# Optimization experiments

Hardware: AMD Instinct MI355X
Metric: run time of the kernel (lower is better)

## Reference

```python
import jax, jax.numpy as jnp
import numpy as np

D = 1024
H = 16
HD = D // H
L = 2048
B = 1
MLP = 8192
ROPE_BASE = 10000.0
LN_EPS = 1e-5


def layer_norm(x):
    mu = jnp.mean(x, axis=-1, keepdims=True)
    var = jnp.var(x, axis=-1, keepdims=True)
    return (x - mu) / jnp.sqrt(var + LN_EPS)


def rope(x):
    # x: [B, H, L, HD]; non-traditional (rotate-half / NeoX style)
    half = HD // 2
    inv_freq = 1.0 / (ROPE_BASE ** (jnp.arange(0, half, dtype=jnp.float32) / half))
    pos = jnp.arange(x.shape[2], dtype=jnp.float32)
    ang = pos[:, None] * inv_freq[None, :]            # [L, half]
    cos, sin = jnp.cos(ang), jnp.sin(ang)
    x1, x2 = x[..., :half], x[..., half:]
    return jnp.concatenate([x1 * cos - x2 * sin, x2 * cos + x1 * sin], axis=-1).astype(x.dtype)


def setup_inputs() -> dict:
    key = jax.random.key(0)
    ks = jax.random.split(key, 5)
    x = jax.random.normal(ks[0], (B, L, D), dtype=jnp.float32)
    # causal additive mask
    neg = jnp.finfo(jnp.float32).min
    mask = jnp.where(jnp.tril(jnp.ones((L, L), dtype=bool)), 0.0, neg).astype(jnp.float32)
    W_attn = jax.random.normal(ks[1], (3 * D, D), dtype=jnp.float32) * (D ** -0.5)
    W_out = jax.random.normal(ks[2], (D, D), dtype=jnp.float32) * (D ** -0.5)
    W_ffp = jax.random.normal(ks[3], (MLP, D), dtype=jnp.float32) * (D ** -0.5)
    W_ffo = jax.random.normal(ks[4], (D, MLP // 2), dtype=jnp.float32) * ((MLP // 2) ** -0.5)
    return {"x": x, "mask": mask, "W_attn": W_attn, "W_out": W_out, "W_ffp": W_ffp, "W_ffo": W_ffo}


def block(x, mask, W_attn, W_out, W_ffp, W_ffo):
    b, l, d = x.shape
    scale = HD ** -0.5
    # attention branch
    xn = layer_norm(x)
    qkv = xn @ W_attn.T                                    # [B, L, 3D]
    q, k, v = jnp.split(qkv, 3, axis=-1)
    q = q.reshape(b, l, H, HD).transpose(0, 2, 1, 3)       # [B, H, L, HD]
    k = k.reshape(b, l, H, HD).transpose(0, 2, 1, 3)
    v = v.reshape(b, l, H, HD).transpose(0, 2, 1, 3)
    q = rope(q)
    k = rope(k)
    scores = jnp.einsum('bhqd,bhkd->bhqk', q * scale, k)   # [B, H, L, L]
    scores = scores + mask
    probs = jax.nn.softmax(scores.astype(jnp.float32), axis=-1).astype(scores.dtype)
    attn = jnp.einsum('bhqk,bhkd->bhqd', probs, v)
    attn = attn.transpose(0, 2, 1, 3).reshape(b, l, d)
    r = attn @ W_out.T
    h = x + r
    # SwiGLU MLP branch: split ff_proj output, swiglu(x2, x1) = silu(x2) * x1
    g = layer_norm(h) @ W_ffp.T                            # [B, L, MLP]
    x1, x2 = jnp.split(g, 2, axis=-1)
    mlp = (jax.nn.silu(x2) * x1) @ W_ffo.T
    return h + mlp


def reference(x, mask, W_attn, W_out, W_ffp, W_ffo):
    return block(x, mask, W_attn, W_out, W_ffp, W_ffo)
```

## Files before the change

### kernel.cpp

```cpp
#include <hip/hip_runtime.h>
#include <math.h>

#define DMODEL 1024
#define NHEAD  16
#define HDIM   64
#define SEQ    2048
#define MLPD   8192
#define HALF_MLP 4096
static constexpr float LN_EPS_C = 1e-5f;
#define NEG_BIG (-1e30f)
#define SM_SHIFT 16.0f

typedef short bf16x8 __attribute__((ext_vector_type(8)));
typedef float f32x4  __attribute__((ext_vector_type(4)));

__device__ __forceinline__ unsigned short f2b(float f) {
    unsigned int u = __float_as_uint(f);
    u = (u + 0x7FFFu + ((u >> 16) & 1u)) >> 16;
    return (unsigned short)u;
}
__device__ __forceinline__ float b2f(unsigned short h) {
    return __uint_as_float((unsigned int)h << 16);
}

__device__ __forceinline__ void async_copy16(const unsigned short* g, unsigned short* l) {
    __builtin_amdgcn_global_load_lds(
        (const __attribute__((address_space(1))) unsigned int*)(g),
        (__attribute__((address_space(3))) unsigned int*)(l),
        16, 0, 0);
}

__global__ void prep_all(const float* __restrict__ x,
                         const float* __restrict__ W_attn, const float* __restrict__ W_out,
                         const float* __restrict__ W_ffp,  const float* __restrict__ W_ffo,
                         unsigned short* __restrict__ xnb, float2* __restrict__ ct,
                         unsigned short* __restrict__ oa, unsigned short* __restrict__ ob,
                         unsigned short* __restrict__ oc, unsigned short* __restrict__ od) {
    const int bid = blockIdx.x;
    const int tid = threadIdx.x;
    if (bid < SEQ) {
        __shared__ float rs[256], rs2[256];
        float4 v = *(const float4*)(x + (size_t)bid * DMODEL + tid * 4);
        rs[tid]  = v.x + v.y + v.z + v.w;
        rs2[tid] = v.x * v.x + v.y * v.y + v.z * v.z + v.w * v.w;
        __syncthreads();
        for (int off = 128; off > 0; off >>= 1) {
            if (tid < off) { rs[tid] += rs[tid + off]; rs2[tid] += rs2[tid + off]; }
            __syncthreads();
        }
        float mu  = rs[0] * (1.0f / DMODEL);
        float var = rs2[0] * (1.0f / DMODEL) - mu * mu;
        float inv = rsqrtf(var + LN_EPS_C);
        ushort4 o;
        o.x = f2b((v.x - mu) * inv); o.y = f2b((v.y - mu) * inv);
        o.z = f2b((v.z - mu) * inv); o.w = f2b((v.w - mu) * inv);
        *(ushort4*)(xnb + (size_t)bid * DMODEL + tid * 4) = o;
    } else if (bid < SEQ + 256) {
        int idx = (bid - SEQ) * 256 + tid;
        int pos = idx >> 5, p = idx & 31;
        float invf = powf(10000.0f, -(float)p / 32.0f);
        float ang = (float)pos * invf;
        ct[idx] = make_float2(cosf(ang), sinf(ang));
    } else {
        const int n1 = 3 * DMODEL * DMODEL;
        const int n2 = n1 + DMODEL * DMODEL;
        const int n3 = n2 + MLPD * DMODEL;
        int i = ((bid - SEQ - 256) * 256 + tid) * 4;
        const float* src; unsigned short* dst; int off;
        if (i < n1)      { src = W_attn; dst = oa; off = i; }
        else if (i < n2) { src = W_out;  dst = ob; off = i - n1; }
        else if (i < n3) {
            src = W_ffp; off = i - n2;
            int row = off >> 10, col = off & 1023;
            int rp  = (row < HALF_MLP) ? (2 * row) : (2 * (row - HALF_MLP) + 1);
            float4 v = *(const float4*)(src + off);
            ushort4 o;
            o.x = f2b(v.x); o.y = f2b(v.y); o.z = f2b(v.z); o.w = f2b(v.w);
            *(ushort4*)(oc + ((size_t)rp << 10) + col) = o;
            return;
        }
        else             { src = W_ffo; dst = od; off = i - n3; }
        float4 v = *(const float4*)(src + off);
        ushort4 o;
        o.x = f2b(v.x); o.y = f2b(v.y); o.z = f2b(v.z); o.w = f2b(v.w);
        *(ushort4*)(dst + off) = o;
    }
}

__global__ void ln_red2(const float* __restrict__ p0, const float* __restrict__ p1,
                        const float* __restrict__ x, float* __restrict__ h,
                        unsigned short* __restrict__ xnb) {
    const int row = blockIdx.x;
    const int tid = threadIdx.x;
    __shared__ float rs[256], rs2[256];
    const size_t base = (size_t)row * DMODEL + tid * 4;
    float4 a = *(const float4*)(p0 + base);
    float4 b = *(const float4*)(p1 + base);
    float4 r = *(const float4*)(x + base);
    float4 v = { a.x + b.x + r.x, a.y + b.y + r.y, a.z + b.z + r.z, a.w + b.w + r.w };
    *(float4*)(h + base) = v;
    rs[tid]  = v.x + v.y + v.z + v.w;
    rs2[tid] = v.x * v.x + v.y * v.y + v.z * v.z + v.w * v.w;
    __syncthreads();
    for (int off = 128; off > 0; off >>= 1) {
        if (tid < off) { rs[tid] += rs[tid + off]; rs2[tid] += rs2[tid + off]; }
        __syncthreads();
    }
    float mu  = rs[0] * (1.0f / DMODEL);
    float var = rs2[0] * (1.0f / DMODEL) - mu * mu;
    float inv = rsqrtf(var + LN_EPS_C);
    ushort4 o;
    o.x = f2b((v.x - mu) * inv); o.y = f2b((v.y - mu) * inv);
    o.z = f2b((v.z - mu) * inv); o.w = f2b((v.w - mu) * inv);
    *(ushort4*)(xnb + base) = o;
}

__global__ __launch_bounds__(256)
void gemm_qkv(const unsigned short* __restrict__ A, const unsigned short* __restrict__ B,
              const float2* __restrict__ ct,
              unsigned short* __restrict__ Qp, unsigned short* __restrict__ Kp,
              unsigned short* __restrict__ Vt) {
    __shared__ unsigned short As[128 * 32];
    __shared__ unsigned short Bs[128 * 32];
    __shared__ unsigned short St[4][16][72];
    const int tid  = threadIdx.x;
    const int lane = tid & 63;
    const int w    = tid >> 6;
    const int wm   = w >> 1;
    const int wn   = w & 1;
    const int m0   = blockIdx.y * 128;
    const int n0   = blockIdx.x * 128;

    f32x4 acc[4][4] = {};

    const int srow = lane >> 2;
    const int scol = (lane & 3) * 8;
    const unsigned short* Abase = A + (size_t)(m0 + w * 32 + srow) * DMODEL + scol;
    const unsigned short* Bbase = B + (size_t)(n0 + w * 32 + srow) * DMODEL + scol;
    unsigned short* AsW = &As[(w * 32) * 32];
    unsigned short* BsW = &Bs[(w * 32) * 32];

    const int fr = lane & 15;
    const int fk = (lane >> 4) * 8;

    for (int k0 = 0; k0 < DMODEL; k0 += 32) {
        async_copy16(Abase + k0,               AsW);
        async_copy16(Abase + k0 + 16 * DMODEL, AsW + 16 * 32);
        async_copy16(Bbase + k0,               BsW);
        async_copy16(Bbase + k0 + 16 * DMODEL, BsW + 16 * 32);
        __syncthreads();

        bf16x8 af[4], bfr[4];
#pragma unroll
        for (int i = 0; i < 4; ++i)
            af[i] = *(const bf16x8*)(&As[(wm * 64 + i * 16 + fr) * 32 + fk]);
#pragma unroll
        for (int j = 0; j < 4; ++j)
            bfr[j] = *(const bf16x8*)(&Bs[(wn * 64 + j * 16 + fr) * 32 + fk]);
#pragma unroll
        for (int i = 0; i < 4; ++i)
#pragma unroll
            for (int j = 0; j < 4; ++j)
                acc[i][j] = __builtin_amdgcn_mfma_f32_16x16x32_bf16(af[i], bfr[j], acc[i][j], 0, 0, 0);
        __syncthreads();
    }

    const int erow   = (lane >> 4) * 4;
    const int ecol   = lane & 15;
    const int region = blockIdx.x >> 3;
    const int head   = ((n0 + wn * 64) >> 6) & 15;

    if (region == 2) {
        const int sbase = m0 + wm * 64;
        const int dl = lane >> 3;
        const int ch = (lane & 7) * 8;
#pragma unroll
        for (int j = 0; j < 4; ++j) {
#pragma unroll
            for (int i = 0; i < 4; ++i) {
                ushort4 o;
                o.x = f2b(acc[i][j][0]); o.y = f2b(acc[i][j][1]);
                o.z = f2b(acc[i][j][2]); o.w = f2b(acc[i][j][3]);
                *(ushort4*)&St[w][ecol][i * 16 + erow] = o;
            }
#pragma unroll
            for (int p = 0; p < 2; ++p) {
                const int dd = p * 8 + dl;
                bf16x8 v = *(const bf16x8*)&St[w][dd][ch];
                *(bf16x8*)(Vt + ((size_t)head * HDIM + j * 16 + dd) * SEQ + sbase + ch) = v;
            }
        }
    } else {
        unsigned short* P = region ? Kp : Qp;
        const float scale = region ? 1.0f : 0.125f;
        unsigned short* qb = &St[w][erow][0];
#pragma unroll
        for (int i = 0; i < 4; ++i) {
#pragma unroll
            for (int r = 0; r < 4; ++r) {
                const int rowg = m0 + wm * 64 + i * 16 + erow + r;
                const float2* crow = ct + (size_t)rowg * 32;
#pragma unroll
                for (int jj = 0; jj < 2; ++jj) {
                    const float2 cs = crow[jj * 16 + ecol];
                    const float x1 = acc[i][jj][r];
                    const float x2 = acc[i][jj + 2][r];
                    qb[jj * 16 + ecol]      = f2b((x1 * cs.x - x2 * cs.y) * scale);
                    qb[jj * 16 + ecol + 32] = f2b((x2 * cs.x + x1 * cs.y) * scale);
                }
                ushort4 o = *(const ushort4*)&qb[ecol * 4];
                *(ushort4*)(P + ((size_t)head * SEQ + rowg) * HDIM + ecol * 4) = o;
            }
        }
    }
}

__global__ __launch_bounds__(256, 2)
void gemm_mfma_sk(const unsigned short* __restrict__ A, const unsigned short* __restrict__ B,
                  float* __restrict__ P, int Ksub, int lda, int ldb, int ldc) {
    __shared__ __align__(16) unsigned short U[4][2][128 * 32];
    const int tid  = threadIdx.x;
    const int lane = tid & 63;
    const int w    = tid >> 6;
    const int wm   = w >> 1;
    const int wn   = w & 1;
    const int m0   = blockIdx.y * 128;
    const int n0   = blockIdx.x * 128;
    const int kb   = blockIdx.z * Ksub;

    f32x4 acc[4][4] = {};

    const int srow = lane >> 2;
    const int scg  = ((lane & 3) ^ ((lane >> 3) & 3)) * 8;
    const int fr   = lane & 15;
    const int quad = lane >> 4;
    const int rchunk = (quad ^ ((fr >> 1) & 3)) * 8;

#define SK_STAGE(T)                                                           \
    {                                                                         \
        const int kk_ = kb + (T) * 32;                                        \
        const int sl_ = (T) & 3;                                              \
        const unsigned short* ga_ = A + (size_t)(m0 + w * 32 + srow) * lda + kk_ + scg; \
        const unsigned short* gb_ = B + (size_t)(n0 + w * 32 + srow) * ldb + kk_ + scg; \
        unsigned short* la_ = &U[sl_][0][(w * 32) * 32];                      \
        unsigned short* lb_ = &U[sl_][1][(w * 32) * 32];                      \
        async_copy16(ga_,                    la_);                            \
        async_copy16(ga_ + 16 * (size_t)lda, la_ + 16 * 32);                  \
        async_copy16(gb_,                    lb_);                            \
        async_copy16(gb_ + 16 * (size_t)ldb, lb_ + 16 * 32);                  \
    }

    const int NT = Ksub >> 5;
    SK_STAGE(0)
    SK_STAGE(1)
    asm volatile("s_waitcnt vmcnt(4)" ::: "memory");
    __builtin_amdgcn_s_barrier();

    for (int t = 0; t < NT; ++t) {
        if (t + 2 < NT) {
            SK_STAGE(t + 2)
            asm volatile("s_waitcnt vmcnt(8)" ::: "memory");
        } else if (t + 1 < NT) {
            asm volatile("s_waitcnt vmcnt(4)" ::: "memory");
        } else {
            asm volatile("s_waitcnt vmcnt(0)" ::: "memory");
        }
        __builtin_amdgcn_s_barrier();
        __builtin_amdgcn_sched_barrier(0);

        const unsigned short* As_ = &U[t & 3][0][0];
        const unsigned short* Bs_ = &U[t & 3][1][0];
        bf16x8 af[4], bfr[4];
#pragma unroll
        for (int i = 0; i < 4; ++i)
            af[i] = *(const bf16x8*)&As_[(wm * 64 + i * 16 + fr) * 32 + rchunk];
#pragma unroll
        for (int j = 0; j < 4; ++j)
            bfr[j] = *(const bf16x8*)&Bs_[(wn * 64 + j * 16 + fr) * 32 + rchunk];

        __builtin_amdgcn_s_setprio(1);
#pragma unroll
        for (int i = 0; i < 4; ++i)
#pragma unroll
            for (int j = 0; j < 4; ++j)
                acc[i][j] = __builtin_amdgcn_mfma_f32_16x16x32_bf16(af[i], bfr[j], acc[i][j], 0, 0, 0);
        __builtin_amdgcn_s_setprio(0);
    }
#undef SK_STAGE

    float* Pp = P + (size_t)blockIdx.z * SEQ * ldc;
    const int erow = (lane >> 4) * 4;
    const int ecol = lane & 15;
#pragma unroll
    for (int i = 0; i < 4; ++i)
#pragma unroll
        for (int j = 0; j < 4; ++j) {
            const int colg = n0 + wn * 64 + j * 16 + ecol;
#pragma unroll
            for (int r = 0; r < 4; ++r) {
                const int rowg = m0 + wm * 64 + i * 16 + erow + r;
                Pp[(size_t)rowg * ldc + colg] = acc[i][j][r];
            }
        }
}

__global__ void reduce4_kernel(const float* __restrict__ p0, const float* __restrict__ p1,
                               const float* __restrict__ p2, const float* __restrict__ p3,
                               const float* __restrict__ res, float* __restrict__ out) {
    int i = (blockIdx.x * blockDim.x + threadIdx.x) * 4;
    float4 a = *(const float4*)(p0 + i);
    float4 b = *(const float4*)(p1 + i);
    float4 c = *(const float4*)(p2 + i);
    float4 d = *(const float4*)(p3 + i);
    float4 r = *(const float4*)(res + i);
    float4 o = { a.x + b.x + c.x + d.x + r.x, a.y + b.y + c.y + d.y + r.y,
                 a.z + b.z + c.z + d.z + r.z, a.w + b.w + c.w + d.w + r.w };
    *(float4*)(out + i) = o;
}

#define FT  32
#define FNT (DMODEL / FT)
__global__ __launch_bounds__(512, 2)
void gemm_ffp_silu_p(const unsigned short* __restrict__ A,
                     const unsigned short* __restrict__ B,
                     unsigned short* __restrict__ gact) {
    __shared__ __align__(16) unsigned short U[4][2][256 * 32];
    const int tid  = threadIdx.x;
    const int lane = tid & 63;
    const int w    = tid >> 6;
    const int wm   = w >> 2;
    const int wn   = w & 3;
    const int fr   = lane & 15;
    const int quad = lane >> 4;

    const int sid = (blockIdx.x & 7) * 32 + (blockIdx.x >> 3);
    const int tm  = sid & 7;
    const int tn  = sid >> 3;

    const unsigned short* Ag = A + (size_t)(tm * 256) * DMODEL;
    const unsigned short* Bg = B + (size_t)(tn * 256) * DMODEL;

    const int srow = tid >> 2;
    const int scg  = ((tid & 3) ^ ((tid >> 3) & 3)) * 8;
    unsigned short* lba = (unsigned short*)&U[0][0][0] + w * 512;
    unsigned short* lbb = (unsigned short*)&U[0][1][0] + w * 512;

    const int rchunk = (quad ^ ((fr >> 1) & 3)) * 8;

    f32x4 acc[8][4] = {};

#define FFP_STAGE(T)                                                          \
    {                                                                         \
        const int k0_ = (T) * FT;                                             \
        const int sl_ = (T) & 3;                                              \
        const unsigned short* ga_ = Ag + (size_t)srow * DMODEL + k0_ + scg;   \
        const unsigned short* gb_ = Bg + (size_t)srow * DMODEL + k0_ + scg;   \
        unsigned short* la_ = lba + sl_ * 16384;                              \
        unsigned short* lb_ = lbb + sl_ * 16384;                              \
        async_copy16(ga_,                la_);                                \
        async_copy16(ga_ + 128 * DMODEL, la_ + 4096);                         \
        async_copy16(gb_,                lb_);                                \
        async_copy16(gb_ + 128 * DMODEL, lb_ + 4096);                         \
    }

    FFP_STAGE(0)
    FFP_STAGE(1)
    asm volatile("s_waitcnt vmcnt(4)" ::: "memory");
    __builtin_amdgcn_s_barrier();

    for (int t = 0; t < FNT; ++t) {
        if (t + 2 < FNT) {
            FFP_STAGE(t + 2)
            asm volatile("s_waitcnt vmcnt(8)" ::: "memory");
        } else if (t + 1 < FNT) {
            asm volatile("s_waitcnt vmcnt(4)" ::: "memory");
        } else {
            asm volatile("s_waitcnt vmcnt(0)" ::: "memory");
        }
        __builtin_amdgcn_s_barrier();
        __builtin_amdgcn_sched_barrier(0);

        const unsigned short* As_ = &U[t & 3][0][0];
        const unsigned short* Bs_ = &U[t & 3][1][0];
        bf16x8 af[8], bf[4];
#pragma unroll
        for (int i = 0; i < 8; ++i)
            af[i] = *(const bf16x8*)&As_[(wm * 128 + i * 16 + fr) * 32 + rchunk];
#pragma unroll
        for (int j = 0; j < 4; ++j)
            bf[j] = *(const bf16x8*)&Bs_[(wn * 64 + j * 16 + fr) * 32 + rchunk];

        __builtin_amdgcn_s_setprio(1);
#pragma unroll
        for (int i = 0; i < 8; ++i)
#pragma unroll
            for (int j = 0; j < 4; ++j)
                acc[i][j] = __builtin_amdgcn_mfma_f32_16x16x32_bf16(af[i], bf[j], acc[i][j], 0, 0, 0);
        __builtin_amdgcn_s_setprio(0);
    }
#undef FFP_STAGE

    __syncthreads();
    typedef unsigned short StRow[40];
    StRow* Stw = reinterpret_cast<StRow*>(&U[0][0][0]) + (size_t)w * 128;

    const bool evn = (fr & 1) == 0;
#pragma unroll
    for (int i = 0; i < 8; ++i)
#pragma unroll
        for (int j = 0; j < 4; ++j)
#pragma unroll
            for (int r = 0; r < 4; ++r) {
                float own = acc[i][j][r];
                float oth = __shfl_xor(own, 1);
                if (evn) {
                    float sil = oth / (1.0f + __expf(-oth));
                    Stw[i * 16 + quad * 4 + r][j * 8 + (fr >> 1)] = f2b(sil * own);
                }
            }
    {
        const int growb = tm * 256 + wm * 128;
        const int colb  = tn * 128 + wn * 32;
#pragma unroll
        for (int p = 0; p < 2; ++p) {
            const int rl = p * 64 + lane;
            unsigned short* dst = gact + (size_t)(growb + rl) * HALF_MLP + colb;
            bf16x8 v0 = *(const bf16x8*)&Stw[rl][0];
            bf16x8 v1 = *(const bf16x8*)&Stw[rl][8];
            bf16x8 v2 = *(const bf16x8*)&Stw[rl][16];
            bf16x8 v3 = *(const bf16x8*)&Stw[rl][24];
            *(bf16x8*)(dst + 0)  = v0;
            *(bf16x8*)(dst + 8)  = v1;
            *(bf16x8*)(dst + 16) = v2;
            *(bf16x8*)(dst + 24) = v3;
        }
    }
}

__global__ __launch_bounds__(256)
void fattn_blk(const unsigned short* __restrict__ Qp,
               const unsigned short* __restrict__ Kp,
               const unsigned short* __restrict__ Vt,
               unsigned short* __restrict__ out) {
    __shared__ unsigned short Ks[2][64][64];
    __shared__ unsigned short Vs[2][64][64];
    __shared__ unsigned short Ps[4][16][72];
    const int tid  = threadIdx.x;
    const int lane = tid & 63;
    const int w    = tid >> 6;
    const int fr   = lane & 15;
    const int quad = lane >> 4;

    const int f    = blockIdx.x;
    const int head = ((f & 7) << 1) | ((f >> 3) & 1);
    const int ub   = f >> 4;
    const int qb   = (ub & 1) ? (31 - (ub >> 1)) : (ub >> 1);
    const int m0   = qb * 64 + w * 16;

    const unsigned short* Qg = Qp + (size_t)head * SEQ * HDIM;
    const unsigned short* Kg = Kp + (size_t)head * SEQ * HDIM;
    const unsigned short* Vg = Vt + (size_t)head * HDIM * SEQ;

    const int rA = (w << 3) + (lane >> 3);
    const int cg = ((lane & 7) ^ ((lane >> 3) & 7)) << 3;

    bf16x8 qf[2];
#pragma unroll
    for (int kk = 0; kk < 2; ++kk)
        qf[kk] = *(const bf16x8*)(Qg + (size_t)(m0 + fr) * HDIM + kk * 32 + quad * 8);

    bf16x8 ones;
#pragma unroll
    for (int e = 0; e < 8; ++e) ones[e] = (short)0x3F80;

    f32x4 accO[4] = {};
    f32x4 accL = {};

    const int ntiles = qb + 1;

    {
        const unsigned short* gk = Kg + (size_t)rA * HDIM + cg;
        unsigned short* dk = &Ks[0][w << 3][0];
        async_copy16(gk, dk);
        async_copy16(gk + 32 * HDIM, dk + 32 * 64);
        const unsigned short* gv = Vg + (size_t)rA * SEQ + cg;
        unsigned short* dv = &Vs[0][w << 3][0];
        async_copy16(gv, dv);
        async_copy16(gv + 32 * SEQ, dv + 32 * 64);
    }
    __syncthreads();

    int cur = 0;
    for (int t = 0; t < ntiles; ++t) {
        if (t + 1 < ntiles) {
            const int j1 = (t + 1) * 64;
            const unsigned short* gk = Kg + (size_t)(j1 + rA) * HDIM + cg;
            unsigned short* dk = &Ks[cur ^ 1][w << 3][0];
            async_copy16(gk, dk);
            async_copy16(gk + 32 * HDIM, dk + 32 * 64);
            const unsigned short* gv = Vg + (size_t)rA * SEQ + j1 + cg;
            unsigned short* dv = &Vs[cur ^ 1][w << 3][0];
            async_copy16(gv, dv);
            async_copy16(gv + 32 * SEQ, dv + 32 * 64);
        }

        const int j0 = t * 64;
        f32x4 accS[4] = {};
#pragma unroll
        for (int kk = 0; kk < 2; ++kk) {
#pragma unroll
            for (int j = 0; j < 4; ++j) {
                bf16x8 kf = *(const bf16x8*)
                    &Ks[cur][j * 16 + fr][(((kk << 2) + quad) ^ (fr & 7)) << 3];
                accS[j] = __builtin_amdgcn_mfma_f32_16x16x32_bf16(qf[kk], kf, accS[j], 0, 0, 0);
            }
        }

        if (t == ntiles - 1) {
#pragma unroll
            for (int j = 0; j < 4; ++j)
#pragma unroll
                for (int r = 0; r < 4; ++r)
                    if (j0 + j * 16 + fr > m0 + quad * 4 + r) accS[j][r] = NEG_BIG;
        }

#pragma unroll
        for (int j = 0; j < 4; ++j)
#pragma unroll
            for (int r = 0; r < 4; ++r)
                Ps[w][quad * 4 + r][j * 16 + fr] = f2b(__expf(accS[j][r] - SM_SHIFT));

#pragma unroll
        for (int kk = 0; kk < 2; ++kk) {
            bf16x8 pf = *(const bf16x8*)&Ps[w][fr][kk * 32 + quad * 8];
            accL = __builtin_amdgcn_mfma_f32_16x16x32_bf16(pf, ones, accL, 0, 0, 0);
#pragma unroll
            for (int j = 0; j < 4; ++j) {
                bf16x8 vf = *(const bf16x8*)
                    &Vs[cur][j * 16 + fr][(((kk << 2) + quad) ^ (fr & 7)) << 3];
                accO[j] = __builtin_amdgcn_mfma_f32_16x16x32_bf16(pf, vf, accO[j], 0, 0, 0);
            }
        }

        __syncthreads();
        cur ^= 1;
    }

#pragma unroll
    for (int r = 0; r < 4; ++r) {
        const float inv = 1.0f / accL[r];
        const int qrow = m0 + quad * 4 + r;
#pragma unroll
        for (int j = 0; j < 4; ++j)
            out[(size_t)qrow * DMODEL + head * HDIM + j * 16 + fr] = f2b(accO[j][r] * inv);
    }
}

extern "C" void kernel_launch(void* const* d_in, const int* in_sizes, int n_in,
                              void* d_out, int out_size, void* d_ws, size_t ws_size,
                              hipStream_t stream) {
    const float* x      = (const float*)d_in[0];
    const float* W_attn = (const float*)d_in[2];
    const float* W_out  = (const float*)d_in[3];
    const float* W_ffp  = (const float*)d_in[4];
    const float* W_ffo  = (const float*)d_in[5];
    float* out = (float*)d_out;

    char* wsb = (char*)d_ws;
    unsigned short* wb_attn = (unsigned short*)(wsb);
    unsigned short* wb_out  = (unsigned short*)(wsb + (6u  << 20));
    unsigned short* wb_ffp  = (unsigned short*)(wsb + (8u  << 20));
    unsigned short* wb_ffo  = (unsigned short*)(wsb + (24u << 20));
    float*          h       = (float*)(wsb + (32u << 20));
    unsigned short* xnb     = (unsigned short*)(wsb + (40u << 20));
    unsigned short* attnb   = (unsigned short*)(wsb + (44u << 20));
    unsigned short* gact    = (unsigned short*)(wsb + (48u << 20));
    unsigned short* Qp      = (unsigned short*)(wsb + (64u << 20));
    unsigned short* Kp      = (unsigned short*)(wsb + (68u << 20));
    unsigned short* Vt      = (unsigned short*)(wsb + (72u << 20));
    float*          wout_p  = (float*)(wsb + (76u << 20));
    float2*         ct      = (float2*)(wsb + (92u << 20));
    float*          ffo_p   = (float*)(wsb + (64u << 20));

    {
        int f2b_blocks = (3 * DMODEL * DMODEL + DMODEL * DMODEL + MLPD * DMODEL
                          + DMODEL * HALF_MLP) / 4 / 256;
        prep_all<<<SEQ + 256 + f2b_blocks, 256, 0, stream>>>(
            x, W_attn, W_out, W_ffp, W_ffo, xnb, ct,
            wb_attn, wb_out, wb_ffp, wb_ffo);
    }

    gemm_qkv<<<dim3(3 * DMODEL / 128, SEQ / 128), 256, 0, stream>>>(
        xnb, wb_attn, ct, Qp, Kp, Vt);

    fattn_blk<<<512, 256, 0, stream>>>(Qp, Kp, Vt, attnb);

    gemm_mfma_sk<<<dim3(DMODEL / 128, SEQ / 128, 2), 256, 0, stream>>>(
        attnb, wb_out, wout_p, DMODEL / 2, DMODEL, DMODEL, DMODEL);

    ln_red2<<<SEQ, 256, 0, stream>>>(wout_p, wout_p + (size_t)SEQ * DMODEL, x, h, xnb);

    gemm_ffp_silu_p<<<256, 512, 0, stream>>>(xnb, wb_ffp, gact);

    gemm_mfma_sk<<<dim3(DMODEL / 128, SEQ / 128, 4), 256, 0, stream>>>(
        gact, wb_ffo, ffo_p, HALF_MLP / 4, HALF_MLP, HALF_MLP, DMODEL);

    reduce4_kernel<<<SEQ * DMODEL / 4 / 256, 256, 0, stream>>>(
        ffo_p, ffo_p + (size_t)SEQ * DMODEL, ffo_p + 2 * (size_t)SEQ * DMODEL,
        ffo_p + 3 * (size_t)SEQ * DMODEL, h, out);
}
```

Before: 289.7 us.

## Multi-stage async pipeline with swizzled LDS for QKV GEMM

Replaces the single-buffered load/sync/compute loop in the QKV projection GEMM with a 4-slot LDS ring and a prefetch distance of two tiles. Waits now use explicit vmcnt counts and one barrier per iteration instead of two. It also XOR-swizzles the 16-byte chunks in LDS to cut bank conflicts, raises wave priority around the MFMA block, and asks for two blocks per CU through launch bounds. The cost is more shared memory (64KB of staging) and hand-written wait counts that must match the number of outstanding async copies.

```diff
diff --git a/kernel.cpp b/kernel.cpp
--- a/kernel.cpp
+++ b/kernel.cpp
@@ -115,13 +115,12 @@
     *(ushort4*)(xnb + base) = o;
 }
 
-__global__ __launch_bounds__(256)
+__global__ __launch_bounds__(256, 2)
 void gemm_qkv(const unsigned short* __restrict__ A, const unsigned short* __restrict__ B,
               const float2* __restrict__ ct,
               unsigned short* __restrict__ Qp, unsigned short* __restrict__ Kp,
               unsigned short* __restrict__ Vt) {
-    __shared__ unsigned short As[128 * 32];
-    __shared__ unsigned short Bs[128 * 32];
+    __shared__ __align__(16) unsigned short U[4][2][128 * 32];
     __shared__ unsigned short St[4][16][72];
     const int tid  = threadIdx.x;
     const int lane = tid & 63;
@@ -134,36 +133,63 @@
     f32x4 acc[4][4] = {};
 
     const int srow = lane >> 2;
-    const int scol = (lane & 3) * 8;
-    const unsigned short* Abase = A + (size_t)(m0 + w * 32 + srow) * DMODEL + scol;
-    const unsigned short* Bbase = B + (size_t)(n0 + w * 32 + srow) * DMODEL + scol;
-    unsigned short* AsW = &As[(w * 32) * 32];
-    unsigned short* BsW = &Bs[(w * 32) * 32];
-
-    const int fr = lane & 15;
-    const int fk = (lane >> 4) * 8;
-
-    for (int k0 = 0; k0 < DMODEL; k0 += 32) {
-        async_copy16(Abase + k0,               AsW);
-        async_copy16(Abase + k0 + 16 * DMODEL, AsW + 16 * 32);
-        async_copy16(Bbase + k0,               BsW);
-        async_copy16(Bbase + k0 + 16 * DMODEL, BsW + 16 * 32);
-        __syncthreads();
-
+    const int scg  = ((lane & 3) ^ ((lane >> 3) & 3)) * 8;
+    const int fr   = lane & 15;
+    const int quad = lane >> 4;
+    const int rchunk = (quad ^ ((fr >> 1) & 3)) * 8;
+
+#define QKV_STAGE(T)                                                          \
+    {                                                                         \
+        const int kk_ = (T) * 32;                                             \
+        const int sl_ = (T) & 3;                                              \
+        const unsigned short* ga_ = A + (size_t)(m0 + w * 32 + srow) * DMODEL + kk_ + scg; \
+        const unsigned short* gb_ = B + (size_t)(n0 + w * 32 + srow) * DMODEL + kk_ + scg; \
+        unsigned short* la_ = &U[sl_][0][(w * 32) * 32];                      \
+        unsigned short* lb_ = &U[sl_][1][(w * 32) * 32];                      \
+        async_copy16(ga_,               la_);                                 \
+        async_copy16(ga_ + 16 * DMODEL, la_ + 16 * 32);                       \
+        async_copy16(gb_,               lb_);                                 \
+        async_copy16(gb_ + 16 * DMODEL, lb_ + 16 * 32);                       \
+    }
+
+    const int NT = DMODEL >> 5;
+    QKV_STAGE(0)
+    QKV_STAGE(1)
+    asm volatile("s_waitcnt vmcnt(4)" ::: "memory");
+    __builtin_amdgcn_s_barrier();
+
+    for (int t = 0; t < NT; ++t) {
+        if (t + 2 < NT) {
+            QKV_STAGE(t + 2)
+            asm volatile("s_waitcnt vmcnt(8)" ::: "memory");
+        } else if (t + 1 < NT) {
+            asm volatile("s_waitcnt vmcnt(4)" ::: "memory");
+        } else {
+            asm volatile("s_waitcnt vmcnt(0)" ::: "memory");
+        }
+        __builtin_amdgcn_s_barrier();
+        __builtin_amdgcn_sched_barrier(0);
+
+        const unsigned short* As_ = &U[t & 3][0][0];
+        const unsigned short* Bs_ = &U[t & 3][1][0];
         bf16x8 af[4], bfr[4];
 #pragma unroll
         for (int i = 0; i < 4; ++i)
-            af[i] = *(const bf16x8*)(&As[(wm * 64 + i * 16 + fr) * 32 + fk]);
+            af[i] = *(const bf16x8*)&As_[(wm * 64 + i * 16 + fr) * 32 + rchunk];
 #pragma unroll
         for (int j = 0; j < 4; ++j)
-            bfr[j] = *(const bf16x8*)(&Bs[(wn * 64 + j * 16 + fr) * 32 + fk]);
+            bfr[j] = *(const bf16x8*)&Bs_[(wn * 64 + j * 16 + fr) * 32 + rchunk];
+
+        __builtin_amdgcn_s_setprio(1);
 #pragma unroll
         for (int i = 0; i < 4; ++i)
 #pragma unroll
             for (int j = 0; j < 4; ++j)
                 acc[i][j] = __builtin_amdgcn_mfma_f32_16x16x32_bf16(af[i], bfr[j], acc[i][j], 0, 0, 0);
-        __syncthreads();
-    }
+        __builtin_amdgcn_s_setprio(0);
+    }
+#undef QKV_STAGE
+    __syncthreads();
 
     const int erow   = (lane >> 4) * 4;
     const int ecol   = lane & 15;
```

Measured after the change: 280.9 us. 3.0% less time.
